# Performance work log

Measured on AMD Instinct MI355X. Metric: run time of the kernel, lower is better.

The kernel has to match this reference:

```python
import jax, jax.numpy as jnp
import numpy as np

H = 300          # hidden_size
M = 256          # molecules
L = 128          # atoms per molecule (uniform -> pad/unpad is a reshape)
A = 1 + M * L    # atoms incl. zero-padding row 0
NB = 6           # max neighbor bonds per atom
B = 1 + 4 * M * L  # directed bonds incl. zero-padding row 0
ATOM_FDIM = 133
BOND_FDIM = 147
DEPTH = 3


def _lin(key, out_d, in_d):
    return (jax.random.normal(key, (out_d, in_d), jnp.float32) / np.sqrt(in_d)).astype(jnp.float32)


def setup_inputs() -> dict:
    key = jax.random.key(0)
    ks = jax.random.split(key, 24)
    s = 1.0 / np.sqrt(H)
    return {
        "f_atoms": jax.random.normal(ks[0], (A, ATOM_FDIM), jnp.float32),
        "f_bonds": jax.random.normal(ks[1], (B, BOND_FDIM), jnp.float32),
        "a2b": jax.random.randint(ks[2], (A, NB), 0, B),
        "b2a": jax.random.randint(ks[3], (B,), 0, A),
        "b2revb": jax.random.randint(ks[4], (B,), 0, B),
        "W_i_atom": _lin(ks[5], H, ATOM_FDIM),
        "W_i_bond": _lin(ks[6], H, BOND_FDIM),
        "W_h0": _lin(ks[7], H, H),
        "W_h1": _lin(ks[8], H, H),
        "W_lr": _lin(ks[9], H, 3 * H),
        "gru_bias": jax.random.uniform(ks[10], (H,), jnp.float32, -s, s),
        "Wih_f": _lin(ks[11], 3 * H, H),
        "Whh_f": _lin(ks[12], 3 * H, H),
        "bih_f": jax.random.uniform(ks[13], (3 * H,), jnp.float32, -s, s),
        "bhh_f": jax.random.uniform(ks[14], (3 * H,), jnp.float32, -s, s),
        "Wih_b": _lin(ks[15], 3 * H, H),
        "Whh_b": _lin(ks[16], 3 * H, H),
        "bih_b": jax.random.uniform(ks[17], (3 * H,), jnp.float32, -s, s),
        "bhh_b": jax.random.uniform(ks[18], (3 * H,), jnp.float32, -s, s),
        "W_o": _lin(ks[19], H, 2 * H),
        "b_o": jax.random.uniform(ks[20], (H,), jnp.float32, -s, s),
    }


def _gru_dir(x, h0, Wih, Whh, bih, bhh, reverse):
    # x: [M, T, H], h0: [M, H] -> outputs [M, T, H], torch.nn.GRU gate math
    gi_all = jnp.swapaxes(x, 0, 1) @ Wih.T + bih  # [T, M, 3H]

    def step(h, gi):
        gh = h @ Whh.T + bhh
        ir, iz, inn = jnp.split(gi, 3, axis=-1)
        hr, hz, hn = jnp.split(gh, 3, axis=-1)
        r = jax.nn.sigmoid(ir + hr)
        z = jax.nn.sigmoid(iz + hz)
        n = jnp.tanh(inn + r * hn)
        h_new = (1.0 - z) * n + z * h
        return h_new, h_new

    _, ys = jax.lax.scan(step, h0, gi_all, reverse=reverse)
    return jnp.swapaxes(ys, 0, 1)


def reference(f_atoms, f_bonds, a2b, b2a, b2revb, W_i_atom, W_i_bond, W_h0, W_h1,
              W_lr, gru_bias, Wih_f, Whh_f, bih_f, bhh_f, Wih_b, Whh_b, bih_b, bhh_b,
              W_o, b_o):
    relu = jax.nn.relu
    input_atom = relu(f_atoms @ W_i_atom.T)            # [A, H]
    message_atom = input_atom
    input_bond = relu(f_bonds @ W_i_bond.T)            # [B, H]
    message_bond = input_bond

    W_h = [W_h0, W_h1]
    for d in range(DEPTH - 1):
        nei = message_bond[a2b]                        # [A, NB, H] gather
        agg = nei.sum(axis=1) * nei.max(axis=1)        # sum * max aggregation
        message_atom = message_atom + agg
        rev = message_bond[b2revb]                     # [B, H]
        message_bond = message_atom[b2a] - rev
        message_bond = message_bond @ W_h[d].T
        message_bond = relu(input_bond + message_bond)  # dropout p=0

    nei = message_bond[a2b]
    agg = nei.sum(axis=1) * nei.max(axis=1)
    node = jnp.concatenate([agg, message_atom, input_atom], axis=1) @ W_lr.T  # [A, H]

    # BatchGRU: uniform molecule sizes -> pad/unpad is a reshape
    message = relu(node + gru_bias)                    # [A, H]
    msg = message[1:].reshape(M, L, H)
    hid = node[1:].reshape(M, L, H)
    h0 = hid.max(axis=1)                               # [M, H] per-mol max init state
    out_f = _gru_dir(msg, h0, Wih_f, Whh_f, bih_f, bhh_f, reverse=False)
    out_b = _gru_dir(msg, h0, Wih_b, Whh_b, bih_b, bhh_b, reverse=True)
    gru_out = jnp.concatenate([out_f, out_b], axis=-1).reshape(M * L, 2 * H)
    row0 = jnp.concatenate([message[0:1], message[0:1]], axis=1)
    agg2 = jnp.concatenate([row0, gru_out], axis=0)    # [A, 2H]

    atom_hiddens = relu(agg2 @ W_o.T + b_o)            # [A, H]
    mol_vecs = atom_hiddens[1:].reshape(M, L, H).mean(axis=1)  # [M, H]
    return mol_vecs
```

## Files before the change

### kernel.cpp

```cpp
#include <hip/hip_runtime.h>
#include <math.h>

#define HH   300
#define H3   900
#define MMOL 256
#define LATM 128
#define AA   32769
#define NBB  6
#define BBND 131073
#define AFD  133
#define BFD  147
#define MLR  (MMOL * LATM)

static __device__ __forceinline__ float sigm(float x) { return 1.0f / (1.0f + expf(-x)); }

typedef __attribute__((ext_vector_type(8))) short bfrag;
typedef __attribute__((ext_vector_type(4))) float ffrag;

static __device__ __forceinline__ unsigned short f2bf(float x) {
    unsigned u = __float_as_uint(x);
    u += 0x7FFF + ((u >> 16) & 1);
    return (unsigned short)(u >> 16);
}
static __device__ __forceinline__ float bf2f(unsigned short h) {
    return __uint_as_float(((unsigned)h) << 16);
}

template<bool RELU, bool BIAS, bool ACCUM>
__global__ __launch_bounds__(256)
void mfma_gemm(const float* __restrict__ X, int ldx,
               const float* __restrict__ W, int ldw,
               const float* __restrict__ Bias, float* __restrict__ C, int ldc,
               int rows, int N, int K)
{
    __shared__ __align__(16) unsigned short Xp[3][64][40];
    __shared__ __align__(16) unsigned short Wp[3][64][40];
    const int tid  = threadIdx.x;
    const int lane = tid & 63;
    const int wv   = tid >> 6;
    const int row0 = blockIdx.x * 64;
    const int col0 = blockIdx.y * 64;
    const int wr   = (wv >> 1) * 32;
    const int wc   = (wv & 1) * 32;
    const int sr   = tid >> 2;
    const int sk   = (tid & 3) * 8;

    ffrag acc[2][2];
#pragma unroll
    for (int i = 0; i < 2; ++i)
#pragma unroll
        for (int j = 0; j < 2; ++j) acc[i][j] = (ffrag){0.0f, 0.0f, 0.0f, 0.0f};

    for (int k0 = 0; k0 < K; k0 += 32) {
        {
            unsigned short h8[8], m8[8], l8[8];
            int gr = row0 + sr;
#pragma unroll
            for (int i = 0; i < 8; ++i) {
                int k = k0 + sk + i;
                float x = (gr < rows && k < K) ? X[(long)gr * ldx + k] : 0.0f;
                unsigned short h = f2bf(x); float r1 = x - bf2f(h);
                unsigned short m = f2bf(r1); float r2 = r1 - bf2f(m);
                h8[i] = h; m8[i] = m; l8[i] = f2bf(r2);
            }
            *(bfrag*)&Xp[0][sr][sk] = *(bfrag*)h8;
            *(bfrag*)&Xp[1][sr][sk] = *(bfrag*)m8;
            *(bfrag*)&Xp[2][sr][sk] = *(bfrag*)l8;

            int wrow = col0 + sr;
#pragma unroll
            for (int i = 0; i < 8; ++i) {
                int k = k0 + sk + i;
                float x = (wrow < N && k < K) ? W[(long)wrow * ldw + k] : 0.0f;
                unsigned short h = f2bf(x); float r1 = x - bf2f(h);
                unsigned short m = f2bf(r1); float r2 = r1 - bf2f(m);
                h8[i] = h; m8[i] = m; l8[i] = f2bf(r2);
            }
            *(bfrag*)&Wp[0][sr][sk] = *(bfrag*)h8;
            *(bfrag*)&Wp[1][sr][sk] = *(bfrag*)m8;
            *(bfrag*)&Wp[2][sr][sk] = *(bfrag*)l8;
        }
        __syncthreads();

        const int fr = lane & 15;
        const int kb = (lane >> 4) * 8;
        bfrag ax[3][2], bx[3][2];
#pragma unroll
        for (int s = 0; s < 3; ++s)
#pragma unroll
            for (int t2 = 0; t2 < 2; ++t2) {
                ax[s][t2] = *(const bfrag*)&Xp[s][wr + t2 * 16 + fr][kb];
                bx[s][t2] = *(const bfrag*)&Wp[s][wc + t2 * 16 + fr][kb];
            }

#pragma unroll
        for (int st = 0; st < 2; ++st)
#pragma unroll
            for (int ct = 0; ct < 2; ++ct) {
                ffrag a = acc[st][ct];
                a = __builtin_amdgcn_mfma_f32_16x16x32_bf16(ax[1][st], bx[1][ct], a, 0, 0, 0);
                a = __builtin_amdgcn_mfma_f32_16x16x32_bf16(ax[0][st], bx[2][ct], a, 0, 0, 0);
                a = __builtin_amdgcn_mfma_f32_16x16x32_bf16(ax[2][st], bx[0][ct], a, 0, 0, 0);
                a = __builtin_amdgcn_mfma_f32_16x16x32_bf16(ax[0][st], bx[1][ct], a, 0, 0, 0);
                a = __builtin_amdgcn_mfma_f32_16x16x32_bf16(ax[1][st], bx[0][ct], a, 0, 0, 0);
                a = __builtin_amdgcn_mfma_f32_16x16x32_bf16(ax[0][st], bx[0][ct], a, 0, 0, 0);
                acc[st][ct] = a;
            }
        __syncthreads();
    }

    const int orow = (lane >> 4) * 4;
    const int ocol = lane & 15;
#pragma unroll
    for (int st = 0; st < 2; ++st)
#pragma unroll
        for (int ct = 0; ct < 2; ++ct)
#pragma unroll
            for (int rg = 0; rg < 4; ++rg) {
                int gr = row0 + wr + st * 16 + orow + rg;
                int gc = col0 + wc + ct * 16 + ocol;
                if (gr < rows && gc < N) {
                    float v = acc[st][ct][rg];
                    if (BIAS)  v += Bias[gc];
                    if (ACCUM) v += C[(long)gr * ldc + gc];
                    if (RELU)  v = fmaxf(v, 0.0f);
                    C[(long)gr * ldc + gc] = v;
                }
            }
}

__global__ void transposeQ(const float* __restrict__ in, float* __restrict__ out)
{
    long idx = (long)blockIdx.x * blockDim.x + threadIdx.x;
    if (idx >= 270000) return;
    int n = (int)(idx / 300), k = (int)(idx - (long)n * 300);
    out[(long)(k >> 2) * 3600 + n * 4 + (k & 3)] = in[idx];
}

__global__ __launch_bounds__(256)
void vw_hi_gemm(float* __restrict__ P, const float* __restrict__ W, int rows)
{
    __shared__ float Xs[16][132];
    __shared__ float Ws[16][192];
    const int row0 = blockIdx.x * 128;
    const int tid  = threadIdx.x;
    const int tm   = (tid >> 4) * 8;
    const int tn   = (tid & 15) * 4;

    float acc[8][12];
#pragma unroll
    for (int i = 0; i < 8; ++i)
#pragma unroll
        for (int j = 0; j < 12; ++j) acc[i][j] = 0.0f;

    for (int k0 = 0; k0 < 300; k0 += 16) {
        const int rem = 300 - k0;
#pragma unroll
        for (int l = 0; l < 2; ++l) {
            int s = tid + l * 256;
            int r = s >> 2, kq = (s & 3) * 4;
            int gr = row0 + r;
            float v0 = 0, v1 = 0, v2 = 0, v3 = 0;
            if (gr < rows) {
                const float* xp = P + (long)gr * 300 + k0 + kq;
                if (rem >= 16) {
                    float4 t4 = *(const float4*)xp;
                    v0 = t4.x; v1 = t4.y; v2 = t4.z; v3 = t4.w;
                } else {
                    if (kq + 0 < rem) v0 = xp[0];
                    if (kq + 1 < rem) v1 = xp[1];
                    if (kq + 2 < rem) v2 = xp[2];
                    if (kq + 3 < rem) v3 = xp[3];
                }
            }
            Xs[kq + 0][r] = v0; Xs[kq + 1][r] = v1;
            Xs[kq + 2][r] = v2; Xs[kq + 3][r] = v3;
        }
        for (int s = tid; s < 600; s += 256) {
            int r = s >> 2, kq = (s & 3) * 4;
            const float* wp = W + (long)(150 + r) * 300 + k0 + kq;
            float v0 = 0, v1 = 0, v2 = 0, v3 = 0;
            if (rem >= 16) {
                float4 t4 = *(const float4*)wp;
                v0 = t4.x; v1 = t4.y; v2 = t4.z; v3 = t4.w;
            } else {
                if (kq + 0 < rem) v0 = wp[0];
                if (kq + 1 < rem) v1 = wp[1];
                if (kq + 2 < rem) v2 = wp[2];
                if (kq + 3 < rem) v3 = wp[3];
            }
            Ws[kq + 0][r] = v0; Ws[kq + 1][r] = v1;
            Ws[kq + 2][r] = v2; Ws[kq + 3][r] = v3;
        }
        __syncthreads();
#pragma unroll
        for (int kk = 0; kk < 16; ++kk) {
            float4 xa = *(const float4*)&Xs[kk][tm];
            float4 xb = *(const float4*)&Xs[kk][tm + 4];
            float4 w0 = *(const float4*)&Ws[kk][tn];
            float4 w1 = *(const float4*)&Ws[kk][tn + 64];
            float4 w2 = *(const float4*)&Ws[kk][tn + 128];
            float xr[8] = {xa.x, xa.y, xa.z, xa.w, xb.x, xb.y, xb.z, xb.w};
            float wr[12] = {w0.x, w0.y, w0.z, w0.w, w1.x, w1.y, w1.z, w1.w,
                            w2.x, w2.y, w2.z, w2.w};
#pragma unroll
            for (int i = 0; i < 8; ++i)
#pragma unroll
                for (int j = 0; j < 12; ++j)
                    acc[i][j] += xr[i] * wr[j];
        }
        __syncthreads();
    }

#pragma unroll
    for (int i = 0; i < 8; ++i) {
        int gr = row0 + tm + i;
        if (gr >= rows) continue;
#pragma unroll
        for (int c = 0; c < 3; ++c)
#pragma unroll
            for (int j = 0; j < 4; ++j) {
                int cn = tn + c * 64 + j;
                if (cn < 150) P[(long)gr * 300 + cn] = acc[i][c * 4 + j];
            }
    }
}

__global__ __launch_bounds__(256)
void bond_half(const float* __restrict__ FB, const float* __restrict__ WiB,
               const float* __restrict__ Th, const float* __restrict__ Vsrc, int vstride,
               const int* __restrict__ b2a, const int* __restrict__ b2revb,
               float* __restrict__ P, int c0, int rows)
{
    __shared__ float Xs[16][132];
    __shared__ float Ws[16][68];
    __shared__ int ra[128], rb[128];
    const int row0 = blockIdx.x * 128;
    const int col0 = blockIdx.y * 64;
    const int tid  = threadIdx.x;

    if (tid < 128) {
        int gr = row0 + tid;
        ra[tid] = (gr < rows) ? b2a[gr] : 0;
    } else {
        int m = tid - 128;
        int gr = row0 + m;
        rb[m] = (gr < rows) ? b2revb[gr] : 0;
    }

    const int tm = (tid >> 4) * 8;
    const int tn = (tid & 15) * 4;
    float acc[8][4];
#pragma unroll
    for (int i = 0; i < 8; ++i)
#pragma unroll
        for (int j = 0; j < 4; ++j) acc[i][j] = 0.0f;

    for (int k0 = 0; k0 < BFD; k0 += 16) {
        const int rem = BFD - k0;
#pragma unroll
        for (int l = 0; l < 2; ++l) {
            int s = tid + l * 256;
            int r = s >> 2, kq = (s & 3) * 4;
            int gr = row0 + r;
            float v0 = 0, v1 = 0, v2 = 0, v3 = 0;
            if (gr < rows) {
                const float* xp = FB + (long)gr * BFD + k0 + kq;
                if (kq + 0 < rem) v0 = xp[0];
                if (kq + 1 < rem) v1 = xp[1];
                if (kq + 2 < rem) v2 = xp[2];
                if (kq + 3 < rem) v3 = xp[3];
            }
            Xs[kq + 0][r] = v0; Xs[kq + 1][r] = v1;
            Xs[kq + 2][r] = v2; Xs[kq + 3][r] = v3;
        }
        {
            int r = tid >> 2, kq = (tid & 3) * 4;
            int gc = col0 + r;
            float v0 = 0, v1 = 0, v2 = 0, v3 = 0;
            if (gc < 150) {
                const float* wp = WiB + (long)(c0 + gc) * BFD + k0 + kq;
                if (kq + 0 < rem) v0 = wp[0];
                if (kq + 1 < rem) v1 = wp[1];
                if (kq + 2 < rem) v2 = wp[2];
                if (kq + 3 < rem) v3 = wp[3];
            }
            Ws[kq + 0][r] = v0; Ws[kq + 1][r] = v1;
            Ws[kq + 2][r] = v2; Ws[kq + 3][r] = v3;
        }
        __syncthreads();
#pragma unroll
        for (int kk = 0; kk < 16; ++kk) {
            float4 xa = *(const float4*)&Xs[kk][tm];
            float4 xb = *(const float4*)&Xs[kk][tm + 4];
            float4 wq = *(const float4*)&Ws[kk][tn];
            float xr[8] = {xa.x, xa.y, xa.z, xa.w, xb.x, xb.y, xb.z, xb.w};
            float wr[4] = {wq.x, wq.y, wq.z, wq.w};
#pragma unroll
            for (int i = 0; i < 8; ++i)
#pragma unroll
                for (int j = 0; j < 4; ++j)
                    acc[i][j] += xr[i] * wr[j];
        }
        __syncthreads();
    }

#pragma unroll
    for (int i = 0; i < 8; ++i) {
        int gr = row0 + tm + i;
        if (gr >= rows) continue;
        int a  = ra[tm + i];
        int rv = rb[tm + i];
#pragma unroll
        for (int j = 0; j < 4; ++j) {
            int cn = col0 + tn + j;
            if (cn >= 150) continue;
            float ib = fmaxf(acc[i][j], 0.0f);
            float v  = ib + Th[(long)a * 150 + cn] - Vsrc[(long)rv * vstride + cn];
            P[(long)gr * 300 + c0 + cn] = fmaxf(v, 0.0f);
        }
    }
}

template<bool ADD>
__global__ void aggregate(const float* __restrict__ mb, const int* __restrict__ a2b,
                          float* __restrict__ dst)
{
    long idx = (long)blockIdx.x * blockDim.x + threadIdx.x;
    if (idx >= (long)AA * HH) return;
    int a = (int)(idx / HH);
    int h = (int)(idx - (long)a * HH);
    const int* nb = a2b + (long)a * NBB;
    float s = 0.0f, mx = -INFINITY;
#pragma unroll
    for (int i = 0; i < NBB; ++i) {
        float v = mb[(long)nb[i] * HH + h];
        s += v;
        mx = fmaxf(mx, v);
    }
    float r = s * mx;
    if (ADD) r += dst[idx];
    dst[idx] = r;
}

__global__ void msgx_kernel(const float* __restrict__ node, const float* __restrict__ gbias,
                            float* __restrict__ msgx)
{
    long idx = (long)blockIdx.x * blockDim.x + threadIdx.x;
    if (idx >= (long)MLR * HH) return;
    int h = (int)(idx % HH);
    msgx[idx] = fmaxf(node[idx + HH] + gbias[h], 0.0f);
}

__global__ void h0_kernel(const float* __restrict__ node, float* __restrict__ hf)
{
    int idx = blockIdx.x * blockDim.x + threadIdx.x;
    if (idx >= MMOL * HH) return;
    int m = idx / HH;
    int h = idx - m * HH;
    long base = (long)(1 + m * LATM) * HH + h;
    float mx = -INFINITY;
    for (int t = 0; t < LATM; ++t) mx = fmaxf(mx, node[base + (long)t * HH]);
    hf[idx] = mx;
}

__global__ __launch_bounds__(1024)
void gru_scan3(const float* __restrict__ WQ_f, const float* __restrict__ bhh_f,
               const float* __restrict__ WQ_b, const float* __restrict__ bhh_b,
               const float* __restrict__ h0, float* __restrict__ gi_f,
               float* __restrict__ gi_b)
{
    const int bid  = blockIdx.x;
    const int xcd  = bid & 7;
    const int dir  = (xcd >= 4) ? 1 : 0;
    const int rank = (bid >> 3) * 4 + (xcd & 3);
    const int m0   = rank * 2;
    const float* WQ  = dir ? WQ_b  : WQ_f;
    const float* bhh = dir ? bhh_b : bhh_f;
    float*       gi  = dir ? gi_b  : gi_f;
    const int tid = threadIdx.x;

    __shared__ float hs[2][304];
    __shared__ float ghs[2][H3];

    float bb = (tid < H3) ? bhh[tid] : 0.0f;

    for (int i = tid; i < 150; i += 1024) {
        int mm = i / 75, q = (i - mm * 75) * 4;
        *(float4*)&hs[mm][q] = *(const float4*)&h0[(long)(m0 + mm) * HH + q];
    }
    __syncthreads();

    for (int s = 0; s < LATM; ++s) {
        const int t = dir ? (LATM - 1 - s) : s;

        if (tid < H3) {
            float a0 = 0.0f, a1 = 0.0f;
            const float* wq = WQ + (long)tid * 4;
#pragma unroll 4
            for (int k0 = 0; k0 < HH; k0 += 4) {
                float4 w = *(const float4*)wq;
                wq += 3600;
                float4 h0v = *(const float4*)&hs[0][k0];
                float4 h1v = *(const float4*)&hs[1][k0];
                a0 += h0v.x * w.x + h0v.y * w.y + h0v.z * w.z + h0v.w * w.w;
                a1 += h1v.x * w.x + h1v.y * w.y + h1v.z * w.z + h1v.w * w.w;
            }
            ghs[0][tid] = a0 + bb;
            ghs[1][tid] = a1 + bb;
        }
        __syncthreads();

        if (tid < 2 * HH) {
            int mm = tid / HH, hh = tid - mm * HH;
            long row = (long)(m0 + mm) * LATM + t;
            float* g = gi + row * H3;
            float ir = g[hh], iz = g[HH + hh], inn = g[2 * HH + hh];
            float r  = sigm(ir + ghs[mm][hh]);
            float z  = sigm(iz + ghs[mm][HH + hh]);
            float nn = tanhf(inn + r * ghs[mm][2 * HH + hh]);
            float hn = (1.0f - z) * nn + z * hs[mm][hh];
            hs[mm][hh] = hn;
            g[hh] = hn;
        }
        __syncthreads();
    }
}

__global__ void mean_kernel(const float* __restrict__ ah, float* __restrict__ out)
{
    int idx = blockIdx.x * blockDim.x + threadIdx.x;
    if (idx >= MMOL * HH) return;
    int m = idx / HH;
    int j = idx - m * HH;
    long base = (long)m * LATM * HH + j;
    float s = 0.0f;
    for (int t = 0; t < LATM; ++t) s += ah[base + (long)t * HH];
    out[idx] = s * (1.0f / LATM);
}

static inline int cdiv(long a, long b) { return (int)((a + b - 1) / b); }

extern "C" void kernel_launch(void* const* d_in, const int* in_sizes, int n_in,
                              void* d_out, int out_size, void* d_ws, size_t ws_size,
                              hipStream_t stream)
{
    const float* f_atoms  = (const float*)d_in[0];
    const float* f_bonds  = (const float*)d_in[1];
    const int*   a2b      = (const int*)d_in[2];
    const int*   b2a      = (const int*)d_in[3];
    const int*   b2revb   = (const int*)d_in[4];
    const float* W_i_atom = (const float*)d_in[5];
    const float* W_i_bond = (const float*)d_in[6];
    const float* W_h0     = (const float*)d_in[7];
    const float* W_h1     = (const float*)d_in[8];
    const float* W_lr     = (const float*)d_in[9];
    const float* gru_bias = (const float*)d_in[10];
    const float* Wih_f    = (const float*)d_in[11];
    const float* Whh_f    = (const float*)d_in[12];
    const float* bih_f    = (const float*)d_in[13];
    const float* bhh_f    = (const float*)d_in[14];
    const float* Wih_b    = (const float*)d_in[15];
    const float* Whh_b    = (const float*)d_in[16];
    const float* bih_b    = (const float*)d_in[17];
    const float* bhh_b    = (const float*)d_in[18];
    const float* W_o      = (const float*)d_in[19];
    const float* b_o      = (const float*)d_in[20];
    float* out = (float*)d_out;

    const size_t NEED = 295530016;
    if (ws_size < NEED) return;

    char* b = (char*)d_ws;
    float* P   = (float*)b;
    float* S   = (float*)(b + 157287600);
    float* MA  = (float*)(b + 235931408);
    float* TH  = (float*)(b + 275254208);

    float* Pia  = P + (size_t)AA * HH;
    float* giF  = (float*)b;
    float* giB  = (float*)(b + 117964800);
    float* MSGX = MA;
    float* AH   = MA;
    float* H0   = TH;
    float* WQ_f = TH + 76800;
    float* WQ_b = TH + 346800;

    dim3 blk(256);
    const int gA = cdiv((long)AA * HH, 256);
    dim3 gmB1(cdiv(BBND, 128), cdiv(150, 64));
    dim3 mIA(cdiv(AA, 64),   5);
    dim3 mIB(cdiv(BBND, 64), 5);
    dim3 mVL(cdiv(BBND, 64), 3);
    dim3 mT (cdiv(AA, 64),   3);
    dim3 mGI(cdiv(MLR, 64),  15);
    dim3 mO (cdiv(MLR, 64),  5);

    mfma_gemm<true, false, false><<<mIA, blk, 0, stream>>>(
        f_atoms, AFD, W_i_atom, AFD, nullptr, MA, HH, AA, HH, AFD);
    mfma_gemm<true, false, false><<<mIB, blk, 0, stream>>>(
        f_bonds, BFD, W_i_bond, BFD, nullptr, P, HH, BBND, HH, BFD);

    const float* Wh[2] = { W_h0, W_h1 };
    for (int d = 0; d < 2; ++d) {
        const float* W = Wh[d];
        aggregate<true><<<gA, blk, 0, stream>>>(P, a2b, MA);
        mfma_gemm<false, false, false><<<mVL, blk, 0, stream>>>(
            P, HH, W, HH, nullptr, S, 150, BBND, 150, HH);
        vw_hi_gemm<<<cdiv(BBND, 128), blk, 0, stream>>>(P, W, BBND);
        mfma_gemm<false, false, false><<<mT, blk, 0, stream>>>(
            MA, HH, W + 150 * HH, HH, nullptr, TH, 150, AA, 150, HH);
        bond_half<<<gmB1, blk, 0, stream>>>(
            f_bonds, W_i_bond, TH, P, 300, b2a, b2revb, P, 150, BBND);
        mfma_gemm<false, false, false><<<mT, blk, 0, stream>>>(
            MA, HH, W, HH, nullptr, TH, 150, AA, 150, HH);
        bond_half<<<gmB1, blk, 0, stream>>>(
            f_bonds, W_i_bond, TH, S, 150, b2a, b2revb, P, 0, BBND);
    }

    aggregate<false><<<gA, blk, 0, stream>>>(P, a2b, S);

    mfma_gemm<true, false, false><<<mIA, blk, 0, stream>>>(
        f_atoms, AFD, W_i_atom, AFD, nullptr, Pia, HH, AA, HH, AFD);
    mfma_gemm<false, false, false><<<mIA, blk, 0, stream>>>(
        S,   HH, W_lr,          H3, nullptr, P, HH, AA, HH, HH);
    mfma_gemm<false, false, true><<<mIA, blk, 0, stream>>>(
        MA,  HH, W_lr + HH,     H3, nullptr, P, HH, AA, HH, HH);
    mfma_gemm<false, false, true><<<mIA, blk, 0, stream>>>(
        Pia, HH, W_lr + 2 * HH, H3, nullptr, P, HH, AA, HH, HH);

    msgx_kernel<<<cdiv((long)MLR * HH, 256), blk, 0, stream>>>(P, gru_bias, MSGX);
    h0_kernel<<<cdiv(MMOL * HH, 256), blk, 0, stream>>>(P, H0);
    transposeQ<<<cdiv(270000, 256), blk, 0, stream>>>(Whh_f, WQ_f);
    transposeQ<<<cdiv(270000, 256), blk, 0, stream>>>(Whh_b, WQ_b);

    mfma_gemm<false, true, false><<<mGI, blk, 0, stream>>>(
        MSGX, HH, Wih_f, HH, bih_f, giF, H3, MLR, H3, HH);
    mfma_gemm<false, true, false><<<mGI, blk, 0, stream>>>(
        MSGX, HH, Wih_b, HH, bih_b, giB, H3, MLR, H3, HH);

    gru_scan3<<<dim3(256), dim3(1024), 0, stream>>>(
        WQ_f, bhh_f, WQ_b, bhh_b, H0, giF, giB);

    mfma_gemm<false, false, false><<<mO, blk, 0, stream>>>(
        giF, H3, W_o,      2 * HH, nullptr, AH, HH, MLR, HH, HH);
    mfma_gemm<true, true, true><<<mO, blk, 0, stream>>>(
        giB, H3, W_o + HH, 2 * HH, b_o,     AH, HH, MLR, HH, HH);

    mean_kernel<<<cdiv(MMOL * HH, 256), blk, 0, stream>>>(AH, out);
}
```

Measured before the change: 5.568 ms.

## Pre-split weights into bf16 planes and widen GEMM tiles across full N

Adds a split_w kernel that converts each weight matrix once into three padded bf16 planes (hi/mid/lo), so the GEMM no longer re-splits weights per tile. The new mfma2 kernel reads B fragments directly from global planes and covers up to 5 column tiles per block, so each X tile is split to bf16 once and reused across all output columns instead of once per column block. This removes redundant X conversion and global reads at the cost of more accumulator registers, possibly lower occupancy, uncached-in-LDS weight reads, and extra small split kernel launches.

```diff
diff --git a/kernel.cpp b/kernel.cpp
--- a/kernel.cpp
+++ b/kernel.cpp
@@ -26,30 +26,50 @@
     return __uint_as_float(((unsigned)h) << 16);
 }
 
-template<bool RELU, bool BIAS, bool ACCUM>
+__global__ void split_w(const float* __restrict__ W, int ldw, int koff, int N, int K,
+                        int Npad, int Kpad, unsigned short* __restrict__ planes)
+{
+    long tot = (long)Npad * Kpad;
+    long idx = (long)blockIdx.x * blockDim.x + threadIdx.x;
+    if (idx >= tot) return;
+    int n = (int)(idx / Kpad), k = (int)(idx - (long)n * Kpad);
+    float x = (n < N && k < K) ? W[(long)n * ldw + koff + k] : 0.0f;
+    unsigned short h = f2bf(x); float r1 = x - bf2f(h);
+    unsigned short m = f2bf(r1); float r2 = r1 - bf2f(m);
+    planes[idx] = h;
+    planes[tot + idx] = m;
+    planes[2 * tot + idx] = f2bf(r2);
+}
+
+template<int NCT, bool RELU, bool BIAS, bool ACCUM>
 __global__ __launch_bounds__(256)
-void mfma_gemm(const float* __restrict__ X, int ldx,
-               const float* __restrict__ W, int ldw,
-               const float* __restrict__ Bias, float* __restrict__ C, int ldc,
-               int rows, int N, int K)
+void mfma2(const float* __restrict__ X, int ldx,
+           const unsigned short* __restrict__ Wpl, int wrow0, int Nalloc, int Kpad,
+           const float* __restrict__ Bias, float* __restrict__ C, int ldc,
+           int rows, int N, int K)
 {
     __shared__ __align__(16) unsigned short Xp[3][64][40];
-    __shared__ __align__(16) unsigned short Wp[3][64][40];
     const int tid  = threadIdx.x;
     const int lane = tid & 63;
     const int wv   = tid >> 6;
     const int row0 = blockIdx.x * 64;
-    const int col0 = blockIdx.y * 64;
+    const int colbase = blockIdx.y * (NCT * 64);
     const int wr   = (wv >> 1) * 32;
     const int wc   = (wv & 1) * 32;
     const int sr   = tid >> 2;
     const int sk   = (tid & 3) * 8;
-
-    ffrag acc[2][2];
-#pragma unroll
-    for (int i = 0; i < 2; ++i)
-#pragma unroll
-        for (int j = 0; j < 2; ++j) acc[i][j] = (ffrag){0.0f, 0.0f, 0.0f, 0.0f};
+    const long PS  = (long)Nalloc * Kpad;
+
+    ffrag acc[NCT][2][2];
+#pragma unroll
+    for (int c = 0; c < NCT; ++c)
+#pragma unroll
+        for (int i = 0; i < 2; ++i)
+#pragma unroll
+            for (int j = 0; j < 2; ++j) acc[c][i][j] = (ffrag){0.f, 0.f, 0.f, 0.f};
+
+    const int fr = lane & 15;
+    const int kb = (lane >> 4) * 8;
 
     for (int k0 = 0; k0 < K; k0 += 32) {
         {
@@ -66,67 +86,66 @@
             *(bfrag*)&Xp[0][sr][sk] = *(bfrag*)h8;
             *(bfrag*)&Xp[1][sr][sk] = *(bfrag*)m8;
             *(bfrag*)&Xp[2][sr][sk] = *(bfrag*)l8;
-
-            int wrow = col0 + sr;
-#pragma unroll
-            for (int i = 0; i < 8; ++i) {
-                int k = k0 + sk + i;
-                float x = (wrow < N && k < K) ? W[(long)wrow * ldw + k] : 0.0f;
-                unsigned short h = f2bf(x); float r1 = x - bf2f(h);
-                unsigned short m = f2bf(r1); float r2 = r1 - bf2f(m);
-                h8[i] = h; m8[i] = m; l8[i] = f2bf(r2);
-            }
-            *(bfrag*)&Wp[0][sr][sk] = *(bfrag*)h8;
-            *(bfrag*)&Wp[1][sr][sk] = *(bfrag*)m8;
-            *(bfrag*)&Wp[2][sr][sk] = *(bfrag*)l8;
-        }
-        __syncthreads();
-
-        const int fr = lane & 15;
-        const int kb = (lane >> 4) * 8;
-        bfrag ax[3][2], bx[3][2];
+        }
+        __syncthreads();
+
+        bfrag ax[3][2];
 #pragma unroll
         for (int s = 0; s < 3; ++s)
 #pragma unroll
-            for (int t2 = 0; t2 < 2; ++t2) {
+            for (int t2 = 0; t2 < 2; ++t2)
                 ax[s][t2] = *(const bfrag*)&Xp[s][wr + t2 * 16 + fr][kb];
-                bx[s][t2] = *(const bfrag*)&Wp[s][wc + t2 * 16 + fr][kb];
-            }
-
-#pragma unroll
-        for (int st = 0; st < 2; ++st)
-#pragma unroll
-            for (int ct = 0; ct < 2; ++ct) {
-                ffrag a = acc[st][ct];
-                a = __builtin_amdgcn_mfma_f32_16x16x32_bf16(ax[1][st], bx[1][ct], a, 0, 0, 0);
-                a = __builtin_amdgcn_mfma_f32_16x16x32_bf16(ax[0][st], bx[2][ct], a, 0, 0, 0);
-                a = __builtin_amdgcn_mfma_f32_16x16x32_bf16(ax[2][st], bx[0][ct], a, 0, 0, 0);
-                a = __builtin_amdgcn_mfma_f32_16x16x32_bf16(ax[0][st], bx[1][ct], a, 0, 0, 0);
-                a = __builtin_amdgcn_mfma_f32_16x16x32_bf16(ax[1][st], bx[0][ct], a, 0, 0, 0);
-                a = __builtin_amdgcn_mfma_f32_16x16x32_bf16(ax[0][st], bx[0][ct], a, 0, 0, 0);
-                acc[st][ct] = a;
-            }
+
+#pragma unroll
+        for (int ct = 0; ct < NCT; ++ct) {
+            int prow0 = wrow0 + colbase + ct * 64 + wc + fr;
+            int pr[2];
+            pr[0] = prow0;              if (pr[0] > Nalloc - 1) pr[0] = Nalloc - 1;
+            pr[1] = prow0 + 16;         if (pr[1] > Nalloc - 1) pr[1] = Nalloc - 1;
+            bfrag bx[3][2];
+#pragma unroll
+            for (int s = 0; s < 3; ++s)
+#pragma unroll
+                for (int t2 = 0; t2 < 2; ++t2)
+                    bx[s][t2] = *(const bfrag*)(Wpl + (long)s * PS + (long)pr[t2] * Kpad + k0 + kb);
+
+#pragma unroll
+            for (int st = 0; st < 2; ++st)
+#pragma unroll
+                for (int c2 = 0; c2 < 2; ++c2) {
+                    ffrag a = acc[ct][st][c2];
+                    a = __builtin_amdgcn_mfma_f32_16x16x32_bf16(ax[1][st], bx[1][c2], a, 0, 0, 0);
+                    a = __builtin_amdgcn_mfma_f32_16x16x32_bf16(ax[0][st], bx[2][c2], a, 0, 0, 0);
+                    a = __builtin_amdgcn_mfma_f32_16x16x32_bf16(ax[2][st], bx[0][c2], a, 0, 0, 0);
+                    a = __builtin_amdgcn_mfma_f32_16x16x32_bf16(ax[0][st], bx[1][c2], a, 0, 0, 0);
+                    a = __builtin_amdgcn_mfma_f32_16x16x32_bf16(ax[1][st], bx[0][c2], a, 0, 0, 0);
+                    a = __builtin_amdgcn_mfma_f32_16x16x32_bf16(ax[0][st], bx[0][c2], a, 0, 0, 0);
+                    acc[ct][st][c2] = a;
+                }
+        }
         __syncthreads();
     }
 
     const int orow = (lane >> 4) * 4;
     const int ocol = lane & 15;
 #pragma unroll
-    for (int st = 0; st < 2; ++st)
-#pragma unroll
-        for (int ct = 0; ct < 2; ++ct)
-#pragma unroll
-            for (int rg = 0; rg < 4; ++rg) {
-                int gr = row0 + wr + st * 16 + orow + rg;
-                int gc = col0 + wc + ct * 16 + ocol;
-                if (gr < rows && gc < N) {
-                    float v = acc[st][ct][rg];
-                    if (BIAS)  v += Bias[gc];
-                    if (ACCUM) v += C[(long)gr * ldc + gc];
-                    if (RELU)  v = fmaxf(v, 0.0f);
-                    C[(long)gr * ldc + gc] = v;
+    for (int ct = 0; ct < NCT; ++ct)
+#pragma unroll
+        for (int st = 0; st < 2; ++st)
+#pragma unroll
+            for (int c2 = 0; c2 < 2; ++c2)
+#pragma unroll
+                for (int rg = 0; rg < 4; ++rg) {
+                    int gr = row0 + wr + st * 16 + orow + rg;
+                    int gc = colbase + ct * 64 + wc + c2 * 16 + ocol;
+                    if (gr < rows && gc < N) {
+                        float v = acc[ct][st][c2][rg];
+                        if (BIAS)  v += Bias[gc];
+                        if (ACCUM) v += C[(long)gr * ldc + gc];
+                        if (RELU)  v = fmaxf(v, 0.0f);
+                        C[(long)gr * ldc + gc] = v;
+                    }
                 }
-            }
 }
 
 __global__ void transposeQ(const float* __restrict__ in, float* __restrict__ out)
@@ -476,6 +495,7 @@
     float* S   = (float*)(b + 157287600);
     float* MA  = (float*)(b + 235931408);
     float* TH  = (float*)(b + 275254208);
+    char*  TAIL = b + 294915616;
 
     float* Pia  = P + (size_t)AA * HH;
     float* giF  = (float*)b;
@@ -486,66 +506,84 @@
     float* WQ_f = TH + 76800;
     float* WQ_b = TH + 346800;
 
+    unsigned short* PL_IA = (unsigned short*)TAIL;
+    unsigned short* PL_IB = (unsigned short*)(TAIL + 307200);
+    unsigned short* PL_W  = (unsigned short*)TAIL;
+    char* THsp = ((char*)TH) + 2467200;
+    unsigned short* PL_WIHF = (unsigned short*)THsp;
+    unsigned short* PL_WIHB = (unsigned short*)(THsp + 1843200);
+    unsigned short* PL_WO1  = (unsigned short*)TH;
+    unsigned short* PL_WO2  = (unsigned short*)(((char*)TH) + 614400);
+
     dim3 blk(256);
     const int gA = cdiv((long)AA * HH, 256);
     dim3 gmB1(cdiv(BBND, 128), cdiv(150, 64));
-    dim3 mIA(cdiv(AA, 64),   5);
-    dim3 mIB(cdiv(BBND, 64), 5);
-    dim3 mVL(cdiv(BBND, 64), 3);
-    dim3 mT (cdiv(AA, 64),   3);
-    dim3 mGI(cdiv(MLR, 64),  15);
-    dim3 mO (cdiv(MLR, 64),  5);
-
-    mfma_gemm<true, false, false><<<mIA, blk, 0, stream>>>(
-        f_atoms, AFD, W_i_atom, AFD, nullptr, MA, HH, AA, HH, AFD);
-    mfma_gemm<true, false, false><<<mIB, blk, 0, stream>>>(
-        f_bonds, BFD, W_i_bond, BFD, nullptr, P, HH, BBND, HH, BFD);
+    const int spl_sm = cdiv(320 * 160, 256);
+    const int spl_md = cdiv(320 * 320, 256);
+    const int spl_lg = cdiv(960 * 320, 256);
+
+    split_w<<<spl_sm, blk, 0, stream>>>(W_i_atom, AFD, 0, 300, AFD, 320, 160, PL_IA);
+    split_w<<<spl_sm, blk, 0, stream>>>(W_i_bond, BFD, 0, 300, BFD, 320, 160, PL_IB);
+    mfma2<5, true, false, false><<<dim3(cdiv(AA, 64), 1), blk, 0, stream>>>(
+        f_atoms, AFD, PL_IA, 0, 320, 160, nullptr, MA, HH, AA, HH, AFD);
+    mfma2<5, true, false, false><<<dim3(cdiv(BBND, 64), 1), blk, 0, stream>>>(
+        f_bonds, BFD, PL_IB, 0, 320, 160, nullptr, P, HH, BBND, HH, BFD);
 
     const float* Wh[2] = { W_h0, W_h1 };
     for (int d = 0; d < 2; ++d) {
         const float* W = Wh[d];
+        split_w<<<spl_md, blk, 0, stream>>>(W, HH, 0, 300, 300, 320, 320, PL_W);
         aggregate<true><<<gA, blk, 0, stream>>>(P, a2b, MA);
-        mfma_gemm<false, false, false><<<mVL, blk, 0, stream>>>(
-            P, HH, W, HH, nullptr, S, 150, BBND, 150, HH);
+        mfma2<3, false, false, false><<<dim3(cdiv(BBND, 64), 1), blk, 0, stream>>>(
+            P, HH, PL_W, 0, 320, 320, nullptr, S, 150, BBND, 150, HH);
         vw_hi_gemm<<<cdiv(BBND, 128), blk, 0, stream>>>(P, W, BBND);
-        mfma_gemm<false, false, false><<<mT, blk, 0, stream>>>(
-            MA, HH, W + 150 * HH, HH, nullptr, TH, 150, AA, 150, HH);
+        mfma2<3, false, false, false><<<dim3(cdiv(AA, 64), 1), blk, 0, stream>>>(
+            MA, HH, PL_W, 150, 320, 320, nullptr, TH, 150, AA, 150, HH);
         bond_half<<<gmB1, blk, 0, stream>>>(
             f_bonds, W_i_bond, TH, P, 300, b2a, b2revb, P, 150, BBND);
-        mfma_gemm<false, false, false><<<mT, blk, 0, stream>>>(
-            MA, HH, W, HH, nullptr, TH, 150, AA, 150, HH);
+        mfma2<3, false, false, false><<<dim3(cdiv(AA, 64), 1), blk, 0, stream>>>(
+            MA, HH, PL_W, 0, 320, 320, nullptr, TH, 150, AA, 150, HH);
         bond_half<<<gmB1, blk, 0, stream>>>(
             f_bonds, W_i_bond, TH, S, 150, b2a, b2revb, P, 0, BBND);
     }
 
     aggregate<false><<<gA, blk, 0, stream>>>(P, a2b, S);
 
-    mfma_gemm<true, false, false><<<mIA, blk, 0, stream>>>(
-        f_atoms, AFD, W_i_atom, AFD, nullptr, Pia, HH, AA, HH, AFD);
-    mfma_gemm<false, false, false><<<mIA, blk, 0, stream>>>(
-        S,   HH, W_lr,          H3, nullptr, P, HH, AA, HH, HH);
-    mfma_gemm<false, false, true><<<mIA, blk, 0, stream>>>(
-        MA,  HH, W_lr + HH,     H3, nullptr, P, HH, AA, HH, HH);
-    mfma_gemm<false, false, true><<<mIA, blk, 0, stream>>>(
-        Pia, HH, W_lr + 2 * HH, H3, nullptr, P, HH, AA, HH, HH);
+    split_w<<<spl_sm, blk, 0, stream>>>(W_i_atom, AFD, 0, 300, AFD, 320, 160, PL_IA);
+    mfma2<5, true, false, false><<<dim3(cdiv(AA, 64), 1), blk, 0, stream>>>(
+        f_atoms, AFD, PL_IA, 0, 320, 160, nullptr, Pia, HH, AA, HH, AFD);
+
+    split_w<<<spl_md, blk, 0, stream>>>(W_lr, H3, 0, 300, 300, 320, 320, PL_W);
+    mfma2<5, false, false, false><<<dim3(cdiv(AA, 64), 1), blk, 0, stream>>>(
+        S, HH, PL_W, 0, 320, 320, nullptr, P, HH, AA, HH, HH);
+    split_w<<<spl_md, blk, 0, stream>>>(W_lr, H3, HH, 300, 300, 320, 320, PL_W);
+    mfma2<5, false, false, true><<<dim3(cdiv(AA, 64), 1), blk, 0, stream>>>(
+        MA, HH, PL_W, 0, 320, 320, nullptr, P, HH, AA, HH, HH);
+    split_w<<<spl_md, blk, 0, stream>>>(W_lr, H3, 2 * HH, 300, 300, 320, 320, PL_W);
+    mfma2<5, false, false, true><<<dim3(cdiv(AA, 64), 1), blk, 0, stream>>>(
+        Pia, HH, PL_W, 0, 320, 320, nullptr, P, HH, AA, HH, HH);
 
     msgx_kernel<<<cdiv((long)MLR * HH, 256), blk, 0, stream>>>(P, gru_bias, MSGX);
     h0_kernel<<<cdiv(MMOL * HH, 256), blk, 0, stream>>>(P, H0);
     transposeQ<<<cdiv(270000, 256), blk, 0, stream>>>(Whh_f, WQ_f);
     transposeQ<<<cdiv(270000, 256), blk, 0, stream>>>(Whh_b, WQ_b);
 
-    mfma_gemm<false, true, false><<<mGI, blk, 0, stream>>>(
-        MSGX, HH, Wih_f, HH, bih_f, giF, H3, MLR, H3, HH);
-    mfma_gemm<false, true, false><<<mGI, blk, 0, stream>>>(
-        MSGX, HH, Wih_b, HH, bih_b, giB, H3, MLR, H3, HH);
+    split_w<<<spl_lg, blk, 0, stream>>>(Wih_f, HH, 0, H3, 300, 960, 320, PL_WIHF);
+    split_w<<<spl_lg, blk, 0, stream>>>(Wih_b, HH, 0, H3, 300, 960, 320, PL_WIHB);
+    mfma2<5, false, true, false><<<dim3(cdiv(MLR, 64), 3), blk, 0, stream>>>(
+        MSGX, HH, PL_WIHF, 0, 960, 320, bih_f, giF, H3, MLR, H3, HH);
+    mfma2<5, false, true, false><<<dim3(cdiv(MLR, 64), 3), blk, 0, stream>>>(
+        MSGX, HH, PL_WIHB, 0, 960, 320, bih_b, giB, H3, MLR, H3, HH);
 
     gru_scan3<<<dim3(256), dim3(1024), 0, stream>>>(
         WQ_f, bhh_f, WQ_b, bhh_b, H0, giF, giB);
 
-    mfma_gemm<false, false, false><<<mO, blk, 0, stream>>>(
-        giF, H3, W_o,      2 * HH, nullptr, AH, HH, MLR, HH, HH);
-    mfma_gemm<true, true, true><<<mO, blk, 0, stream>>>(
-        giB, H3, W_o + HH, 2 * HH, b_o,     AH, HH, MLR, HH, HH);
+    split_w<<<spl_md, blk, 0, stream>>>(W_o, 2 * HH, 0,  300, 300, 320, 320, PL_WO1);
+    split_w<<<spl_md, blk, 0, stream>>>(W_o, 2 * HH, HH, 300, 300, 320, 320, PL_WO2);
+    mfma2<5, false, false, false><<<dim3(cdiv(MLR, 64), 1), blk, 0, stream>>>(
+        giF, H3, PL_WO1, 0, 320, 320, nullptr, AH, HH, MLR, HH, HH);
+    mfma2<5, true, true, true><<<dim3(cdiv(MLR, 64), 1), blk, 0, stream>>>(
+        giB, H3, PL_WO2, 0, 320, 320, b_o, AH, HH, MLR, HH, HH);
 
     mean_kernel<<<cdiv(MMOL * HH, 256), blk, 0, stream>>>(AH, out);
 }
```

Measured after the change: 5.355 ms. -3.8%, faster.
